# Performance work log

Measured on AMD Instinct MI355X. Metric: run time of the kernel, lower is better.

The kernel has to match this reference:

```python
import jax, jax.numpy as jnp
import numpy as np

N = 50000   # nodes
E = 1600000 # edges
F = 128     # node feature dim
D_ENC, D_EMB, D_H = 32, 12, 128
TEMPERATURE = 10.0


def _dense(key, fan_in, fan_out):
    kw, kb = jax.random.split(key)
    W = jax.random.normal(kw, (fan_in, fan_out), jnp.float32) * (1.0 / jnp.sqrt(fan_in))
    b = jnp.zeros((fan_out,), jnp.float32)
    return W, b


def setup_inputs() -> dict:
    key = jax.random.key(0)
    ks = jax.random.split(key, 12)
    nodes = jax.random.normal(ks[0], (N, F), jnp.float32)
    senders = jax.random.randint(ks[1], (E,), 0, N, dtype=jnp.int32)
    receivers = jax.random.randint(ks[2], (E,), 0, N, dtype=jnp.int32)
    W_enc, b_enc = _dense(ks[3], F, D_ENC)
    W_inf, b_inf = _dense(ks[4], D_ENC + 1, 1)
    W_emb, b_emb = _dense(ks[5], F, D_EMB)
    W1, b1 = _dense(ks[6], D_EMB, D_H)
    W2, b2 = _dense(ks[7], D_H, D_H)
    Wy, by = _dense(ks[8], D_H, 1)
    Wx, bx = _dense(ks[9], D_H, 4)
    return {"nodes": nodes, "senders": senders, "receivers": receivers,
            "W_enc": W_enc, "b_enc": b_enc, "W_inf": W_inf, "b_inf": b_inf,
            "W_emb": W_emb, "b_emb": b_emb, "W1": W1, "b1": b1,
            "W2": W2, "b2": b2, "Wy": Wy, "by": by, "Wx": Wx, "bx": bx}


def reference(nodes, senders, receivers, W_enc, b_enc, W_inf, b_inf,
              W_emb, b_emb, W1, b1, W2, b2, Wy, by, Wx, bx):
    n_nodes = nodes.shape[0]
    # EncodeNet: Dense(32) + relu
    vodes = jax.nn.relu(nodes @ W_enc + b_enc)                      # [N, 32]
    # compute_pure_message: gather by senders, scatter-add by receivers
    msg = jax.ops.segment_sum(vodes[senders], receivers, num_segments=n_nodes)
    vodes = vodes + msg                                             # [N, 32]
    # concat last raw node feature
    vodes = jnp.concatenate([vodes, nodes[:, -1:]], axis=1)         # [N, 33]
    # InfluenceNet: Dense(1), softmax over nodes
    influence = vodes @ W_inf + b_inf                               # [N, 1]
    attention = jax.nn.softmax(influence, axis=0)                   # [N, 1]
    # EmbedNet: Dense(12); softmax-weighted pooling over nodes
    emb = nodes @ W_emb + b_emb                                     # [N, 12]
    g = jnp.sum(emb * attention, axis=0)                            # [12]
    # ActNet head
    h = jax.nn.relu(g @ W1 + b1)
    h = jax.nn.relu(h @ W2 + b2)
    value = h @ Wy + by                                             # [1]
    logits = h @ Wx + bx                                            # [4]
    return (logits / TEMPERATURE, value)
```

## Files before the change

### kernel.cpp

```cpp
#include <hip/hip_runtime.h>
#include <hip/hip_bf16.h>


#define NF 128
#define DENC 32
#define DEMB 12
#define DH 128

#define NSLICE 128
#define NRANGE 4
#define R_SCAT 16000
#define ROWB (NSLICE*64)

template <int NJ, int LDW>
__device__ __forceinline__ void gemv_rows(
    const float4* __restrict__ x4p, const float* __restrict__ W,
    int jbase, const float* __restrict__ bias, float* acc, float& x_last)
{
#pragma unroll
    for (int j = 0; j < NJ; j++) acc[j] = bias[jbase + j];
#pragma unroll 2
    for (int c = 0; c < 8; c++) {
        float4 xa = x4p[4 * c + 0];
        float4 xb = x4p[4 * c + 1];
        float4 xc = x4p[4 * c + 2];
        float4 xd = x4p[4 * c + 3];
        float xs[16] = {xa.x, xa.y, xa.z, xa.w, xb.x, xb.y, xb.z, xb.w,
                        xc.x, xc.y, xc.z, xc.w, xd.x, xd.y, xd.z, xd.w};
#pragma unroll
        for (int u = 0; u < 16; u++) {
            const int k = 16 * c + u;
#pragma unroll
            for (int j = 0; j < NJ; j++)
                acc[j] = fmaf(xs[u], W[k * LDW + jbase + j], acc[j]);
        }
        if (c == 7) x_last = xd.w;
    }
}

__global__ __launch_bounds__(256) void k1_node(
    const float* __restrict__ nodes,
    const float* __restrict__ W_enc, const float* __restrict__ b_enc,
    const float* __restrict__ W_inf, const float* __restrict__ b_inf,
    const float* __restrict__ W_emb, const float* __restrict__ b_emb,
    float* __restrict__ p, float* __restrict__ inflb, float* __restrict__ embT,
    int n_nodes)
{
    __shared__ float tabp[3][64];
    const int tid  = threadIdx.x;
    const int lane = tid & 63;
    const int wv   = __builtin_amdgcn_readfirstlane(tid >> 6);
    const int node = blockIdx.x * 64 + lane;
    const bool ok  = (node < n_nodes);

    const float4* x4p = ok ? (const float4*)(nodes + (size_t)node * NF)
                           : (const float4*)nodes;

    float x127 = 0.f;
    if (wv == 3) {
        float acc[DEMB];
        gemv_rows<DEMB, DEMB>(x4p, W_emb, 0, b_emb, acc, x127);
        if (ok) {
#pragma unroll
            for (int j = 0; j < DEMB; j++)
                embT[(size_t)j * n_nodes + node] = acc[j];
        }
    } else {
        const int jbase = __builtin_amdgcn_readfirstlane(wv * 11);
        float pp = 0.f;
        if (wv == 2) {
            float acc[10];
            gemv_rows<10, DENC>(x4p, W_enc, jbase, b_enc, acc, x127);
#pragma unroll
            for (int j = 0; j < 10; j++)
                pp += fmaxf(acc[j], 0.f) * W_inf[jbase + j];
        } else {
            float acc[11];
            gemv_rows<11, DENC>(x4p, W_enc, jbase, b_enc, acc, x127);
#pragma unroll
            for (int j = 0; j < 11; j++)
                pp += fmaxf(acc[j], 0.f) * W_inf[jbase + j];
        }
        tabp[wv][lane] = pp;
    }
    __syncthreads();

    if (wv == 0 && ok) {
        float pn = tabp[0][lane] + tabp[1][lane] + tabp[2][lane];
        p[node] = pn;
        inflb[node] = pn + x127 * W_inf[DENC] + b_inf[0];
    }
}

__global__ __launch_bounds__(512) void k2_scatter(
    const int* __restrict__ senders, const int* __restrict__ recvs,
    const float* __restrict__ p, float* __restrict__ rep2,
    int n_nodes, int n_edges)
{
    __shared__ float tab[R_SCAT];
    const int slice = blockIdx.x >> 2;
    const int rng_i = blockIdx.x & 3;
    const int e0 = (int)((long long)n_edges * slice / NSLICE);
    const int e1 = (int)((long long)n_edges * (slice + 1) / NSLICE);
    const int lo = rng_i * R_SCAT;
    const int rng = min(R_SCAT, n_nodes - lo);

    float4* tab4 = (float4*)tab;
    for (int i = threadIdx.x; i < (rng + 3) / 4; i += 512)
        tab4[i] = make_float4(0.f, 0.f, 0.f, 0.f);
    __syncthreads();

    const int ae0 = (e0 + 3) & ~3;
    const int ae1 = e1 & ~3;
    for (int e = e0 + (int)threadIdx.x; e < ae0; e += 512) {
        unsigned rr = (unsigned)(recvs[e] - lo);
        if (rr < (unsigned)rng) atomicAdd(&tab[rr], p[senders[e]]);
    }
    const int4* r4 = (const int4*)recvs;
    const int4* s4 = (const int4*)senders;
    for (int i = ae0 / 4 + (int)threadIdx.x; i < ae1 / 4; i += 512) {
        int4 r = r4[i];
        int4 s = s4[i];
        unsigned rr;
        rr = (unsigned)(r.x - lo); if (rr < (unsigned)rng) atomicAdd(&tab[rr], p[s.x]);
        rr = (unsigned)(r.y - lo); if (rr < (unsigned)rng) atomicAdd(&tab[rr], p[s.y]);
        rr = (unsigned)(r.z - lo); if (rr < (unsigned)rng) atomicAdd(&tab[rr], p[s.z]);
        rr = (unsigned)(r.w - lo); if (rr < (unsigned)rng) atomicAdd(&tab[rr], p[s.w]);
    }
    for (int e = ae1 + (int)threadIdx.x; e < e1; e += 512) {
        unsigned rr = (unsigned)(recvs[e] - lo);
        if (rr < (unsigned)rng) atomicAdd(&tab[rr], p[senders[e]]);
    }
    __syncthreads();

    float4* dst4 = (float4*)(rep2 + (size_t)(lo >> 6) * ROWB + slice * 64);
    for (int i4 = threadIdx.x; i4 < rng / 4; i4 += 512) {
        const int chunk = i4 >> 4;
        const int col4  = i4 & 15;
        dst4[(size_t)chunk * (ROWB / 4) + col4] = tab4[i4];
    }
    for (int i = (rng & ~3) + threadIdx.x; i < rng; i += 512)
        rep2[(size_t)(lo >> 6) * ROWB + (size_t)(i >> 6) * ROWB
             + slice * 64 + (i & 63)] = tab[i];
}

__global__ __launch_bounds__(256) void k3_soft(
    const float* __restrict__ inflb, const float* __restrict__ rep2,
    const float* __restrict__ embT, float* __restrict__ psum, int n_nodes)
{
    __shared__ float tab[4][64];
    const int tid  = threadIdx.x;
    const int lane = tid & 63;
    const int wv   = __builtin_amdgcn_readfirstlane(tid >> 6);
    const int node = blockIdx.x * 64 + lane;
    const bool ok  = (node < n_nodes);

    {
        const float* base = rep2 + (size_t)blockIdx.x * ROWB + 32 * wv * 64 + lane;
        float s = 0.f;
#pragma unroll 8
        for (int i = 0; i < 32; i++)
            s += base[i * 64];
        tab[wv][lane] = ok ? s : 0.f;
    }
    __syncthreads();

    if (wv == 0) {
        float infl = ok ? inflb[node] + tab[0][lane] + tab[1][lane]
                          + tab[2][lane] + tab[3][lane]
                        : -1e30f;
        float m = infl;
#pragma unroll
        for (int off = 32; off; off >>= 1)
            m = fmaxf(m, __shfl_down(m, off, 64));
        m = __shfl(m, 0, 64);

        const float w = ok ? expf(infl - m) : 0.f;
        float v13[13];
        v13[0] = w;
#pragma unroll
        for (int j = 0; j < DEMB; j++)
            v13[1 + j] = ok ? w * embT[(size_t)j * n_nodes + node] : 0.f;

#pragma unroll
        for (int v = 0; v < 13; v++) {
            float x = v13[v];
#pragma unroll
            for (int off = 32; off; off >>= 1)
                x += __shfl_down(x, off, 64);
            v13[v] = x;
        }
        if (lane == 0) {
            psum[blockIdx.x * 14] = m;
#pragma unroll
            for (int v = 0; v < 13; v++)
                psum[blockIdx.x * 14 + 1 + v] = v13[v];
        }
    }
}

__global__ __launch_bounds__(512, 1) void k4_head(
    const float* __restrict__ psum,
    const float* __restrict__ W1, const float* __restrict__ b1,
    const float* __restrict__ W2, const float* __restrict__ b2,
    const float* __restrict__ Wy, const float* __restrict__ by,
    const float* __restrict__ Wx, const float* __restrict__ bx,
    float* __restrict__ out, int nblk)
{
    const int t  = threadIdx.x;
    const int wv = t >> 6;
    const int ln = t & 63;

    __shared__ float sred[8][14];
    __shared__ float tot[14];
    __shared__ float g[DEMB];
    __shared__ float h1[DH];
    __shared__ float part[4][DH];
    __shared__ float h2[DH];
    __shared__ float wred[8][5];

    float m = -1e30f;
    for (int b = t; b < nblk; b += 512) m = fmaxf(m, psum[b * 14]);
#pragma unroll
    for (int off = 32; off; off >>= 1)
        m = fmaxf(m, __shfl_down(m, off, 64));
    if (ln == 0) sred[wv][0] = m;
    __syncthreads();
    float M = sred[0][0];
#pragma unroll
    for (int i = 1; i < 8; i++) M = fmaxf(M, sred[i][0]);
    __syncthreads();

    float acc[13];
#pragma unroll
    for (int v = 0; v < 13; v++) acc[v] = 0.f;
    for (int b = t; b < nblk; b += 512) {
        float sc = expf(psum[b * 14] - M);
#pragma unroll
        for (int v = 0; v < 13; v++)
            acc[v] = fmaf(sc, psum[b * 14 + 1 + v], acc[v]);
    }
#pragma unroll
    for (int v = 0; v < 13; v++) {
        float x = acc[v];
#pragma unroll
        for (int off = 32; off; off >>= 1)
            x += __shfl_down(x, off, 64);
        if (ln == 0) sred[wv][v] = x;
    }
    __syncthreads();
    if (t < 13) {
        float s = 0.f;
#pragma unroll
        for (int i = 0; i < 8; i++) s += sred[i][t];
        tot[t] = s;
    }
    __syncthreads();
    if (t < DEMB) g[t] = tot[1 + t] / tot[0];
    __syncthreads();

    if (t < DH) {
        float s1 = b1[t];
#pragma unroll
        for (int i = 0; i < DEMB; i++) s1 = fmaf(g[i], W1[i * DH + t], s1);
        h1[t] = fmaxf(s1, 0.f);
    }
    __syncthreads();

    {
        const int o  = t & 127;
        const int ks = t >> 7;
        float s = 0.f;
        const float* w2 = W2 + (size_t)(32 * ks) * DH + o;
#pragma unroll 8
        for (int i = 0; i < 32; i++)
            s = fmaf(h1[32 * ks + i], w2[i * DH], s);
        part[ks][o] = s;
    }
    __syncthreads();
    if (t < DH)
        h2[t] = fmaxf(b2[t] + part[0][t] + part[1][t] + part[2][t] + part[3][t], 0.f);
    __syncthreads();

    if (t < DH) {
        const float v = h2[t];
        float pr[5];
#pragma unroll
        for (int j = 0; j < 4; j++) pr[j] = v * Wx[t * 4 + j];
        pr[4] = v * Wy[t];
#pragma unroll
        for (int j = 0; j < 5; j++) {
            float x = pr[j];
#pragma unroll
            for (int off = 32; off; off >>= 1)
                x += __shfl_down(x, off, 64);
            if (ln == 0) wred[wv][j] = x;
        }
    }
    __syncthreads();
    if (t < 4)
        out[t] = (wred[0][t] + wred[1][t] + bx[t]) / 10.0f;
    else if (t == 4)
        out[4] = wred[0][4] + wred[1][4] + by[0];
}

extern "C" void kernel_launch(void* const* d_in, const int* in_sizes, int n_in,
                              void* d_out, int out_size, void* d_ws, size_t ws_size,
                              hipStream_t stream) {
    const float* nodes   = (const float*)d_in[0];
    const int*   senders = (const int*)d_in[1];
    const int*   recvs   = (const int*)d_in[2];
    const float* W_enc   = (const float*)d_in[3];
    const float* b_enc   = (const float*)d_in[4];
    const float* W_inf   = (const float*)d_in[5];
    const float* b_inf   = (const float*)d_in[6];
    const float* W_emb   = (const float*)d_in[7];
    const float* b_emb   = (const float*)d_in[8];
    const float* W1      = (const float*)d_in[9];
    const float* b1      = (const float*)d_in[10];
    const float* W2      = (const float*)d_in[11];
    const float* b2      = (const float*)d_in[12];
    const float* Wy      = (const float*)d_in[13];
    const float* by      = (const float*)d_in[14];
    const float* Wx      = (const float*)d_in[15];
    const float* bx      = (const float*)d_in[16];
    float* out = (float*)d_out;

    const int n_nodes = in_sizes[0] / NF;
    const int n_edges = in_sizes[1];
    const int nb64 = (n_nodes + 63) / 64;

    float* ws    = (float*)d_ws;
    float* p     = ws;
    float* inflb = ws + n_nodes;
    float* embT  = ws + 2 * (size_t)n_nodes;
    float* rep2  = ws + 14 * (size_t)n_nodes;
    float* psum  = rep2 + (size_t)nb64 * ROWB;

    hipLaunchKernelGGL(k1_node, dim3(nb64), dim3(256), 0, stream,
                       nodes, W_enc, b_enc, W_inf, b_inf, W_emb, b_emb,
                       p, inflb, embT, n_nodes);
    hipLaunchKernelGGL(k2_scatter, dim3(NSLICE * NRANGE), dim3(512), 0, stream,
                       senders, recvs, p, rep2, n_nodes, n_edges);
    hipLaunchKernelGGL(k3_soft, dim3(nb64), dim3(256), 0, stream,
                       inflb, rep2, embT, psum, n_nodes);
    hipLaunchKernelGGL(k4_head, dim3(1), dim3(512), 0, stream,
                       psum, W1, b1, W2, b2, Wy, by, Wx, bx, out, nb64);
}
```

Before: 155.9 us.

## Halve scatter node ranges with larger LDS tables and vectorize partial-sum reduction

The scatter kernel now splits nodes into 2 ranges of about 25k entries instead of 4 of 16k, using dynamic shared memory and 1024-thread blocks. Each edge slice therefore re-reads the edge arrays half as often. The write-out now uses global chunk indexing, so range boundaries no longer have to be multiples of 64. The softmax kernel reduces the per-slice partials with float4 loads and cross-lane shuffles instead of scalar strided loads. The trade-off is fewer blocks (256) with larger LDS use, which may lower occupancy and raise atomic contention per block.

```diff
diff --git a/kernel.cpp b/kernel.cpp
--- a/kernel.cpp
+++ b/kernel.cpp
@@ -8,8 +8,8 @@
 #define DH 128
 
 #define NSLICE 128
-#define NRANGE 4
-#define R_SCAT 16000
+#define NRANGE 2
+#define R_SCAT 25024
 #define ROWB (NSLICE*64)
 
 template <int NJ, int LDW>
@@ -92,33 +92,33 @@
     }
 }
 
-__global__ __launch_bounds__(512) void k2_scatter(
+__global__ __launch_bounds__(1024) void k2_scatter(
     const int* __restrict__ senders, const int* __restrict__ recvs,
     const float* __restrict__ p, float* __restrict__ rep2,
     int n_nodes, int n_edges)
 {
-    __shared__ float tab[R_SCAT];
-    const int slice = blockIdx.x >> 2;
-    const int rng_i = blockIdx.x & 3;
+    extern __shared__ float tab[];
+    const int slice = blockIdx.x >> 1;
+    const int rng_i = blockIdx.x & 1;
     const int e0 = (int)((long long)n_edges * slice / NSLICE);
     const int e1 = (int)((long long)n_edges * (slice + 1) / NSLICE);
     const int lo = rng_i * R_SCAT;
     const int rng = min(R_SCAT, n_nodes - lo);
 
     float4* tab4 = (float4*)tab;
-    for (int i = threadIdx.x; i < (rng + 3) / 4; i += 512)
+    for (int i = threadIdx.x; i < (rng + 3) / 4; i += 1024)
         tab4[i] = make_float4(0.f, 0.f, 0.f, 0.f);
     __syncthreads();
 
     const int ae0 = (e0 + 3) & ~3;
     const int ae1 = e1 & ~3;
-    for (int e = e0 + (int)threadIdx.x; e < ae0; e += 512) {
+    for (int e = e0 + (int)threadIdx.x; e < ae0; e += 1024) {
         unsigned rr = (unsigned)(recvs[e] - lo);
         if (rr < (unsigned)rng) atomicAdd(&tab[rr], p[senders[e]]);
     }
     const int4* r4 = (const int4*)recvs;
     const int4* s4 = (const int4*)senders;
-    for (int i = ae0 / 4 + (int)threadIdx.x; i < ae1 / 4; i += 512) {
+    for (int i = ae0 / 4 + (int)threadIdx.x; i < ae1 / 4; i += 1024) {
         int4 r = r4[i];
         int4 s = s4[i];
         unsigned rr;
@@ -127,21 +127,23 @@
         rr = (unsigned)(r.z - lo); if (rr < (unsigned)rng) atomicAdd(&tab[rr], p[s.z]);
         rr = (unsigned)(r.w - lo); if (rr < (unsigned)rng) atomicAdd(&tab[rr], p[s.w]);
     }
-    for (int e = ae1 + (int)threadIdx.x; e < e1; e += 512) {
+    for (int e = ae1 + (int)threadIdx.x; e < e1; e += 1024) {
         unsigned rr = (unsigned)(recvs[e] - lo);
         if (rr < (unsigned)rng) atomicAdd(&tab[rr], p[senders[e]]);
     }
     __syncthreads();
 
-    float4* dst4 = (float4*)(rep2 + (size_t)(lo >> 6) * ROWB + slice * 64);
-    for (int i4 = threadIdx.x; i4 < rng / 4; i4 += 512) {
-        const int chunk = i4 >> 4;
-        const int col4  = i4 & 15;
-        dst4[(size_t)chunk * (ROWB / 4) + col4] = tab4[i4];
-    }
-    for (int i = (rng & ~3) + threadIdx.x; i < rng; i += 512)
-        rep2[(size_t)(lo >> 6) * ROWB + (size_t)(i >> 6) * ROWB
-             + slice * 64 + (i & 63)] = tab[i];
+    const int g4base = lo >> 2;
+    for (int i4 = threadIdx.x; i4 < rng / 4; i4 += 1024) {
+        const int g4    = g4base + i4;
+        const int chunk = g4 >> 4;
+        const int col4  = g4 & 15;
+        ((float4*)rep2)[(size_t)chunk * (ROWB / 4) + slice * 16 + col4] = tab4[i4];
+    }
+    for (int i = (rng & ~3) + threadIdx.x; i < rng; i += 1024) {
+        const int g = lo + i;
+        rep2[(size_t)(g >> 6) * ROWB + slice * 64 + (g & 63)] = tab[i];
+    }
 }
 
 __global__ __launch_bounds__(256) void k3_soft(
@@ -156,12 +158,29 @@
     const bool ok  = (node < n_nodes);
 
     {
-        const float* base = rep2 + (size_t)blockIdx.x * ROWB + 32 * wv * 64 + lane;
-        float s = 0.f;
-#pragma unroll 8
-        for (int i = 0; i < 32; i++)
-            s += base[i * 64];
-        tab[wv][lane] = ok ? s : 0.f;
+        const float* chunk = rep2 + (size_t)blockIdx.x * ROWB;
+        const int s0 = lane >> 4;
+        const int c4 = lane & 15;
+        float4 a = make_float4(0.f, 0.f, 0.f, 0.f);
+#pragma unroll
+        for (int i = 0; i < 8; i++) {
+            const int slice = 32 * wv + s0 + 4 * i;
+            float4 v = ((const float4*)(chunk + slice * 64))[c4];
+            a.x += v.x; a.y += v.y; a.z += v.z; a.w += v.w;
+        }
+#pragma unroll
+        for (int off = 16; off <= 32; off <<= 1) {
+            a.x += __shfl_xor(a.x, off, 64);
+            a.y += __shfl_xor(a.y, off, 64);
+            a.z += __shfl_xor(a.z, off, 64);
+            a.w += __shfl_xor(a.w, off, 64);
+        }
+        if (s0 == 0) {
+            tab[wv][4 * c4 + 0] = a.x;
+            tab[wv][4 * c4 + 1] = a.y;
+            tab[wv][4 * c4 + 2] = a.z;
+            tab[wv][4 * c4 + 3] = a.w;
+        }
     }
     __syncthreads();
 
@@ -337,10 +356,15 @@
     float* rep2  = ws + 14 * (size_t)n_nodes;
     float* psum  = rep2 + (size_t)nb64 * ROWB;
 
+    (void)hipFuncSetAttribute((const void*)k2_scatter,
+                              hipFuncAttributeMaxDynamicSharedMemorySize,
+                              R_SCAT * (int)sizeof(float));
+
     hipLaunchKernelGGL(k1_node, dim3(nb64), dim3(256), 0, stream,
                        nodes, W_enc, b_enc, W_inf, b_inf, W_emb, b_emb,
                        p, inflb, embT, n_nodes);
-    hipLaunchKernelGGL(k2_scatter, dim3(NSLICE * NRANGE), dim3(512), 0, stream,
+    hipLaunchKernelGGL(k2_scatter, dim3(NSLICE * NRANGE), dim3(1024),
+                       R_SCAT * sizeof(float), stream,
                        senders, recvs, p, rep2, n_nodes, n_edges);
     hipLaunchKernelGGL(k3_soft, dim3(nb64), dim3(256), 0, stream,
                        inflb, rep2, embT, psum, n_nodes);
```

Result: faster. 152.3 us, median of 2 (-2.3%).
